# Kernel optimization log

Measured on AMD Instinct MI355X. Metric: run time of the kernel, lower is better.

Reference implementation:

```python
import jax, jax.numpy as jnp
import numpy as np

NEG_SLOPE = 0.01  # F.leaky_relu default
N_NODES = 50000
N_EDGES = 800000
DIMS = [1, 64, 128, 64, 1]


def _lrelu(x):
    return jnp.where(x >= 0, x, NEG_SLOPE * x)


def _gconv(x, src, dst, W, b, n):
    # DGL GraphConv, norm='none': sum-aggregate src features into dst, then linear.
    # (DGL multiplies first when in_feats > out_feats; identical math since sum is linear.)
    if x.shape[1] > W.shape[1]:
        x = x @ W
        return jax.ops.segment_sum(x[src], dst, num_segments=n) + b
    agg = jax.ops.segment_sum(x[src], dst, num_segments=n)  # [n, d_in]
    return agg @ W + b


def setup_inputs() -> dict:
    key = jax.random.key(0)
    ks = jax.random.split(key, 16)
    inp = {
        "in_feat": jax.random.normal(ks[0], (N_NODES, 1), jnp.float32),
        "src": jax.random.randint(ks[1], (N_EDGES,), 0, N_NODES),
        "dst": jax.random.randint(ks[2], (N_EDGES,), 0, N_NODES),
    }
    for i in range(4):
        fi, fo = DIMS[i], DIMS[i + 1]
        scale = (2.0 / (fi + fo)) ** 0.5  # xavier-style
        inp[f"W{i}"] = jax.random.normal(ks[3 + 2 * i], (fi, fo), jnp.float32) * scale
        inp[f"b{i}"] = jax.random.normal(ks[4 + 2 * i], (fo,), jnp.float32) * 0.01
    return inp


def reference(in_feat, src, dst, W0, b0, W1, b1, W2, b2, W3, b3):
    n = in_feat.shape[0]
    h = _lrelu(_gconv(in_feat, src, dst, W0, b0, n))
    h = _lrelu(_gconv(h, src, dst, W1, b1, n))
    h = _lrelu(_gconv(h, src, dst, W2, b2, n))
    h = _lrelu(_gconv(h, src, dst, W3, b3, n))
    return h[1]  # node index 1, shape (1,)
```

## Files before the change

### kernel.cpp

```cpp
#include <hip/hip_runtime.h>

#define N_NODES 50000
#define N_EDGES 800000
#define NE4 (N_EDGES / 4)
#define NMASKW 1568
#define C1MAX 64
#define CAP   16
#define S2MAX 1024
#define DMAX  4096
#define BK    96
#define SB1   ((NE4 + 255) / 256)
#define FGRID 256
#define SUBW  64

#define AS(p, v)  __hip_atomic_store((p), (v), __ATOMIC_RELAXED, __HIP_MEMORY_SCOPE_AGENT)
#define ALD(p)    __hip_atomic_load((p), __ATOMIC_RELAXED, __HIP_MEMORY_SCOPE_AGENT)
#define AADD(p,v) __hip_atomic_fetch_add((p), (v), __ATOMIC_RELAXED, __HIP_MEMORY_SCOPE_AGENT)

__device__ __forceinline__ float lrelu(float v) { return v >= 0.f ? v : 0.01f * v; }
__device__ __forceinline__ bool mtest(const unsigned int* m, int i) {
    return (m[i >> 5] >> (i & 31)) & 1u;
}

__global__ __launch_bounds__(256) void scan1_k(const int4* __restrict__ dst4,
                                               const int* __restrict__ src,
                                               int* __restrict__ e1cnt, int* __restrict__ e1val,
                                               unsigned int* __restrict__ zbase, int zwords) {
    __shared__ int lcnt;
    __shared__ int lval[CAP];
    const int tid = threadIdx.x;
    const int t = blockIdx.x * 256 + tid;
    if (tid == 0) lcnt = 0;
    __syncthreads();
    if (t < zwords) zbase[t] = 0u;
    if (t < NE4) {
        int4 d4 = dst4[t];
        int dv[4] = { d4.x, d4.y, d4.z, d4.w };
#pragma unroll
        for (int k = 0; k < 4; ++k) {
            if (dv[k] == 1) {
                int q = atomicAdd(&lcnt, 1);
                if (q < CAP) lval[q] = src[t * 4 + k];
            }
        }
    }
    __syncthreads();
    int c = lcnt < CAP ? lcnt : CAP;
    if (tid == 0) e1cnt[blockIdx.x] = c;
    if (tid < c) e1val[blockIdx.x * CAP + tid] = lval[tid];
}

__global__ __launch_bounds__(256) void scan2_k(const int4* __restrict__ dst4,
                                               const int* __restrict__ src,
                                               const int* __restrict__ e1cnt,
                                               const int* __restrict__ e1val,
                                               unsigned int* __restrict__ f2m,
                                               int* __restrict__ pos2, int* __restrict__ cnt2,
                                               int2* __restrict__ eD, int* __restrict__ cntD) {
    __shared__ unsigned int msk[NMASKW];
    __shared__ int candN[C1MAX];
    __shared__ int candC;
    const int tid = threadIdx.x;
    for (int k = tid; k < NMASKW; k += 256) msk[k] = 0u;
    if (tid == 0) candC = 0;
    __syncthreads();
    for (int b = tid; b < SB1; b += 256) {
        int c = e1cnt[b]; if (c > CAP) c = CAP;
        for (int i = 0; i < c; ++i) {
            int n = e1val[b * CAP + i];
            unsigned int bit = 1u << (n & 31);
            unsigned int old = atomicOr(&msk[n >> 5], bit);
            if (!(old & bit)) { int q = atomicAdd(&candC, 1); if (q < C1MAX) candN[q] = n; }
        }
    }
    __syncthreads();
    int c1 = candC; if (c1 > C1MAX) c1 = C1MAX;
    int t = blockIdx.x * 256 + tid;
    if (t >= NE4) return;
    int4 d4 = dst4[t];
    int dv[4] = { d4.x, d4.y, d4.z, d4.w };
#pragma unroll
    for (int k = 0; k < 4; ++k) {
        int dd = dv[k];
        if (mtest(msk, dd)) {
            int ss = src[t * 4 + k];
            unsigned int bit = 1u << (ss & 31);
            unsigned int old = atomicOr(&f2m[ss >> 5], bit);
            if (!(old & bit)) {
                int q2 = atomicAdd(cnt2, 1);
                if (q2 < S2MAX) AS(&pos2[ss], q2);
            }
            int r = 0;
            for (int u = 0; u < c1; ++u) r += (candN[u] < dd);
            int q = atomicAdd(cntD, 1);
            if (q < DMAX) {
                unsigned long long ev = (unsigned long long)(unsigned int)ss |
                                        ((unsigned long long)(unsigned int)r << 32);
                AS((unsigned long long*)&eD[q], ev);
            }
        }
    }
}

__global__ __launch_bounds__(256) void scan3_k(const int4* __restrict__ dst4,
                                               const int* __restrict__ src,
                                               const unsigned int* __restrict__ f2m,
                                               unsigned int* __restrict__ f3m,
                                               const int* __restrict__ pos2,
                                               float* __restrict__ agg0,
                                               int* __restrict__ bucket,
                                               int* __restrict__ slotCnt) {
    __shared__ unsigned int msk[NMASKW];
    const int tid = threadIdx.x;
    for (int k = tid; k < NMASKW; k += 256) msk[k] = f2m[k];
    __syncthreads();
    int t = blockIdx.x * 256 + tid;
    if (t >= NE4) return;
    int4 d4 = dst4[t];
    int dv[4] = { d4.x, d4.y, d4.z, d4.w };
#pragma unroll
    for (int k = 0; k < 4; ++k) {
        int dd = dv[k];
        if (mtest(msk, dd)) {
            int ss = src[t * 4 + k];
            unsigned int bit = 1u << (ss & 31);
            unsigned int old = atomicOr(&f3m[ss >> 5], bit);
            if (!(old & bit)) AS(&agg0[ss], 0.f);
            int sl = pos2[dd];
            if ((unsigned)sl < S2MAX) {
                int bi = atomicAdd(&slotCnt[sl], 1);
                if (bi < BK) AS(&bucket[sl * BK + bi], ss);
            }
        }
    }
}

struct P8 {
    const int4* dst4; const int4* src4; const float* x;
    const unsigned int* f3m; float* agg0;
    const int2* eD; const int* cntD; const int* pos2; int2* eDr;
    const int* bucket; const int* slotCnt; const int* cnt2;
    const int* e1cnt; const int* e1val;
    const float* W0; const float* b0; const float* W1; const float* b1;
    const float* W2; const float* b2; const float* W3; const float* b3;
    float* gacc; int* sub; int* top; int* rel; int* subB; int* topB; float* out;
};

__global__ __launch_bounds__(256) void fused8_k(P8 p) {
    __shared__ unsigned int msk[NMASKW];
    __shared__ float xv[128];
    __shared__ float part[256];
    __shared__ float rowA[64];
    __shared__ float rowH[128];
    __shared__ float rowT[64];
    __shared__ float t3s[C1MAX];
    __shared__ int candN[C1MAX];
    __shared__ int candC;
    __shared__ int lflag;
    const int tid = threadIdx.x;
    const int gid = blockIdx.x * 256 + tid;
    const int g = tid >> 6, j = tid & 63;

    int cD = *p.cntD; if (cD > DMAX) cD = DMAX;
    if (gid < cD) {
        int2 e = p.eD[gid];
        int sl = p.pos2[e.x];
        unsigned long long ev =
            (unsigned long long)(unsigned int)((unsigned)sl < S2MAX ? sl : -1) |
            ((unsigned long long)(unsigned int)e.y << 32);
        AS((unsigned long long*)&p.eDr[gid], ev);
    }
    for (int k = tid; k < NMASKW; k += 256) msk[k] = p.f3m[k];
    __syncthreads();
    for (int t = gid; t < NE4; t += FGRID * 256) {
        int4 d4 = p.dst4[t];
        bool m0 = mtest(msk, d4.x), m1 = mtest(msk, d4.y);
        bool m2 = mtest(msk, d4.z), m3 = mtest(msk, d4.w);
        if (m0 | m1 | m2 | m3) {
            int4 s4 = p.src4[t];
            if (m0) atomicAdd(&p.agg0[d4.x], p.x[s4.x]);
            if (m1) atomicAdd(&p.agg0[d4.y], p.x[s4.y]);
            if (m2) atomicAdd(&p.agg0[d4.z], p.x[s4.z]);
            if (m3) atomicAdd(&p.agg0[d4.w], p.x[s4.w]);
        }
    }
    __syncthreads();
    if (tid == 0) {
        int s = blockIdx.x & 7;
        int old = AADD(&p.sub[s * SUBW], 1);
        if (old == (FGRID / 8) - 1) {
            int o2 = AADD(p.top, 1);
            if (o2 == 7) AS(p.rel, 1);
        }
        while (ALD(p.rel) == 0) __builtin_amdgcn_s_sleep(8);
    }
    __syncthreads();

    int c2 = *p.cnt2; if (c2 > S2MAX) c2 = S2MAX;
    const float w0 = p.W0[j], bb0 = p.b0[j];
    for (int b = blockIdx.x; b < c2; b += FGRID) {
        int cnt = p.slotCnt[b]; if (cnt > BK) cnt = BK;
        if (tid < cnt) xv[tid] = p.agg0[p.bucket[b * BK + tid]];
        __syncthreads();
        float racc = 0.f;
        for (int m = g; m < cnt; m += 4) racc += lrelu(xv[m] * w0 + bb0);
        part[tid] = racc;
        __syncthreads();
        if (tid < 64)
            rowA[tid] = part[tid] + part[64 + tid] + part[128 + tid] + part[192 + tid];
        __syncthreads();
        if (tid < 128) {
            float h = p.b1[tid];
#pragma unroll
            for (int k = 0; k < 64; ++k) h += rowA[k] * p.W1[k * 128 + tid];
            rowH[tid] = lrelu(h);
        }
        __syncthreads();
        if (tid < 64) {
            float a2 = 0.f;
#pragma unroll
            for (int k = 0; k < 128; ++k) a2 += rowH[k] * p.W2[k * 64 + tid];
            rowT[tid] = a2;
        }
        __syncthreads();
        for (int base = 0; base < cD; base += 256) {
            int i = base + tid;
            int2 e = make_int2(-1, -1);
            if (i < cD) e = p.eDr[i];
            bool m = (e.x == b);
            unsigned long long bal = __ballot(m);
            while (bal) {
                int bit = __builtin_ctzll(bal); bal &= bal - 1;
                int sl1 = __shfl(e.y, bit, 64);
                if ((unsigned)sl1 < C1MAX)
                    atomicAdd(&p.gacc[sl1 * 64 + j], rowT[j]);
            }
        }
        __syncthreads();
    }

    __syncthreads();
    if (tid == 0) {
        lflag = 0;
        int s = blockIdx.x & 7;
        int old = AADD(&p.subB[s * SUBW], 1);
        if (old == (FGRID / 8) - 1) {
            int o2 = AADD(p.topB, 1);
            lflag = (o2 == 7);
        }
    }
    __syncthreads();
    if (!lflag) return;

    for (int k = tid; k < NMASKW; k += 256) msk[k] = 0u;
    if (tid == 0) candC = 0;
    __syncthreads();
    for (int b = tid; b < SB1; b += 256) {
        int c = p.e1cnt[b]; if (c > CAP) c = CAP;
        for (int i = 0; i < c; ++i) {
            int n = p.e1val[b * CAP + i];
            unsigned int bit = 1u << (n & 31);
            unsigned int old = atomicOr(&msk[n >> 5], bit);
            if (!(old & bit)) { int q = atomicAdd(&candC, 1); if (q < C1MAX) candN[q] = n; }
        }
    }
    __syncthreads();
    int c1 = candC; if (c1 > C1MAX) c1 = C1MAX;
    int widx = tid >> 6;
    for (int q = widx; q < c1; q += 4) {
        int n = candN[q];
        int r = 0;
        for (int u = 0; u < c1; ++u) r += (candN[u] < n);
        float v = lrelu(p.gacc[r * 64 + j] + p.b2[j]) * p.W3[j];
        for (int off = 32; off > 0; off >>= 1) v += __shfl_down(v, off, 64);
        if (j == 0) t3s[r] = v;
    }
    __syncthreads();
    float ssum = 0.f;
    for (int b = tid; b < SB1; b += 256) {
        int c = p.e1cnt[b]; if (c > CAP) c = CAP;
        for (int i = 0; i < c; ++i) {
            int n = p.e1val[b * CAP + i];
            int r = 0;
            for (int u = 0; u < c1; ++u) r += (candN[u] < n);
            ssum += t3s[r];
        }
    }
    part[tid] = ssum;
    __syncthreads();
    for (int off = 128; off > 0; off >>= 1) {
        if (tid < off) part[tid] += part[tid + off];
        __syncthreads();
    }
    if (tid == 0) p.out[0] = lrelu(part[0] + p.b3[0]);
}

extern "C" void kernel_launch(void* const* d_in, const int* in_sizes, int n_in,
                              void* d_out, int out_size, void* d_ws, size_t ws_size,
                              hipStream_t stream) {
    const float* x   = (const float*)d_in[0];
    const int*   src = (const int*)d_in[1];
    const int*   dst = (const int*)d_in[2];
    const float* W0 = (const float*)d_in[3];  const float* b0 = (const float*)d_in[4];
    const float* W1 = (const float*)d_in[5];  const float* b1 = (const float*)d_in[6];
    const float* W2 = (const float*)d_in[7];  const float* b2 = (const float*)d_in[8];
    const float* W3 = (const float*)d_in[9];  const float* b3 = (const float*)d_in[10];
    float* out = (float*)d_out;
    const int4* dst4 = (const int4*)dst;
    const int4* src4 = (const int4*)src;

    char* base = (char*)d_ws;
    size_t off = 0;
    auto take = [&](size_t bytes) { char* q = base + off; off += (bytes + 255) & ~(size_t)255; return q; };
    unsigned int* f2m = (unsigned int*)take(NMASKW * 4);
    unsigned int* f3m = (unsigned int*)take(NMASKW * 4);
    int* cnt2  = (int*)take(4);
    int* cntD  = (int*)take(4);
    int* top   = (int*)take(4);
    int* rel   = (int*)take(4);
    int* topB  = (int*)take(4);
    int* sub   = (int*)take((size_t)8 * SUBW * 4);
    int* subB  = (int*)take((size_t)8 * SUBW * 4);
    int* slotCnt = (int*)take((size_t)S2MAX * 4);
    float* gacc  = (float*)take((size_t)C1MAX * 64 * 4);
    int zwords = (int)(off / 4);
    float* agg0   = (float*)take((size_t)N_NODES * 4);
    int*   e1cnt  = (int*)take((size_t)SB1 * 4);
    int*   e1val  = (int*)take((size_t)SB1 * CAP * 4);
    int2*  eD     = (int2*)take((size_t)DMAX * 8);
    int2*  eDr    = (int2*)take((size_t)DMAX * 8);
    int*   bucket = (int*)take((size_t)S2MAX * BK * 4);
    int*   pos2   = (int*)take((size_t)N_NODES * 4);

    scan1_k<<<SB1, 256, 0, stream>>>(dst4, src, e1cnt, e1val, (unsigned int*)base, zwords);
    scan2_k<<<SB1, 256, 0, stream>>>(dst4, src, e1cnt, e1val, f2m, pos2, cnt2, eD, cntD);
    scan3_k<<<SB1, 256, 0, stream>>>(dst4, src, f2m, f3m, pos2, agg0, bucket, slotCnt);

    P8 hp;
    hp.dst4 = dst4; hp.src4 = src4; hp.x = x;
    hp.f3m = f3m; hp.agg0 = agg0;
    hp.eD = eD; hp.cntD = cntD; hp.pos2 = pos2; hp.eDr = eDr;
    hp.bucket = bucket; hp.slotCnt = slotCnt; hp.cnt2 = cnt2;
    hp.e1cnt = e1cnt; hp.e1val = e1val;
    hp.W0 = W0; hp.b0 = b0; hp.W1 = W1; hp.b1 = b1;
    hp.W2 = W2; hp.b2 = b2; hp.W3 = W3; hp.b3 = b3;
    hp.gacc = gacc; hp.sub = sub; hp.top = top; hp.rel = rel;
    hp.subB = subB; hp.topB = topB; hp.out = out;
    fused8_k<<<FGRID, 256, 0, stream>>>(hp);
}
```

Before: 139.4 us.

## Split edge aggregation into separate kernel, replacing in-kernel grid barrier

The layer-0 masked edge aggregation and the eDr remap move out of the fused kernel into a new full-grid kernel, scan4_k. This removes the spin-wait grid barrier that separated that phase from the per-bucket MLP phase. The aggregation now runs with one thread per int4 chunk across all blocks instead of a 256-block grid-stride loop, which should help parallelism. In exchange it adds one kernel launch and its boundary overhead.

```diff
diff --git a/kernel.cpp b/kernel.cpp
--- a/kernel.cpp
+++ b/kernel.cpp
@@ -14,7 +14,6 @@
 #define SUBW  64
 
 #define AS(p, v)  __hip_atomic_store((p), (v), __ATOMIC_RELAXED, __HIP_MEMORY_SCOPE_AGENT)
-#define ALD(p)    __hip_atomic_load((p), __ATOMIC_RELAXED, __HIP_MEMORY_SCOPE_AGENT)
 #define AADD(p,v) __hip_atomic_fetch_add((p), (v), __ATOMIC_RELAXED, __HIP_MEMORY_SCOPE_AGENT)
 
 __device__ __forceinline__ float lrelu(float v) { return v >= 0.f ? v : 0.01f * v; }
@@ -135,18 +134,53 @@
     }
 }
 
-struct P8 {
-    const int4* dst4; const int4* src4; const float* x;
-    const unsigned int* f3m; float* agg0;
-    const int2* eD; const int* cntD; const int* pos2; int2* eDr;
-    const int* bucket; const int* slotCnt; const int* cnt2;
-    const int* e1cnt; const int* e1val;
+__global__ __launch_bounds__(256) void scan4_k(const int4* __restrict__ dst4,
+                                               const int4* __restrict__ src4,
+                                               const float* __restrict__ x,
+                                               const unsigned int* __restrict__ f3m,
+                                               float* __restrict__ agg0,
+                                               const int2* __restrict__ eD,
+                                               const int* __restrict__ cntD,
+                                               const int* __restrict__ pos2,
+                                               int2* __restrict__ eDr) {
+    __shared__ unsigned int msk[NMASKW];
+    int g = blockIdx.x * 256 + threadIdx.x;
+    {
+        int cD = *cntD; if (cD > DMAX) cD = DMAX;
+        if (g < cD) {
+            int2 e = eD[g];
+            int sl = pos2[e.x];
+            unsigned long long ev =
+                (unsigned long long)(unsigned int)((unsigned)sl < S2MAX ? sl : -1) |
+                ((unsigned long long)(unsigned int)e.y << 32);
+            AS((unsigned long long*)&eDr[g], ev);
+        }
+    }
+    for (int k = threadIdx.x; k < NMASKW; k += 256) msk[k] = f3m[k];
+    __syncthreads();
+    if (g >= NE4) return;
+    int4 d4 = dst4[g];
+    bool m0 = mtest(msk, d4.x), m1 = mtest(msk, d4.y);
+    bool m2 = mtest(msk, d4.z), m3 = mtest(msk, d4.w);
+    if (m0 | m1 | m2 | m3) {
+        int4 s4 = src4[g];
+        if (m0) atomicAdd(&agg0[d4.x], x[s4.x]);
+        if (m1) atomicAdd(&agg0[d4.y], x[s4.y]);
+        if (m2) atomicAdd(&agg0[d4.z], x[s4.z]);
+        if (m3) atomicAdd(&agg0[d4.w], x[s4.w]);
+    }
+}
+
+struct P10 {
+    const int* bucket; const int* slotCnt; const float* agg0;
     const float* W0; const float* b0; const float* W1; const float* b1;
     const float* W2; const float* b2; const float* W3; const float* b3;
-    float* gacc; int* sub; int* top; int* rel; int* subB; int* topB; float* out;
+    const int* cnt2; const int2* eDr; const int* cntD;
+    const int* e1cnt; const int* e1val;
+    float* gacc; int* sub; int* top; float* out;
 };
 
-__global__ __launch_bounds__(256) void fused8_k(P8 p) {
+__global__ __launch_bounds__(256) void fused10_k(P10 p) {
     __shared__ unsigned int msk[NMASKW];
     __shared__ float xv[128];
     __shared__ float part[256];
@@ -158,46 +192,11 @@
     __shared__ int candC;
     __shared__ int lflag;
     const int tid = threadIdx.x;
-    const int gid = blockIdx.x * 256 + tid;
     const int g = tid >> 6, j = tid & 63;
-
+    int c2 = *p.cnt2; if (c2 > S2MAX) c2 = S2MAX;
     int cD = *p.cntD; if (cD > DMAX) cD = DMAX;
-    if (gid < cD) {
-        int2 e = p.eD[gid];
-        int sl = p.pos2[e.x];
-        unsigned long long ev =
-            (unsigned long long)(unsigned int)((unsigned)sl < S2MAX ? sl : -1) |
-            ((unsigned long long)(unsigned int)e.y << 32);
-        AS((unsigned long long*)&p.eDr[gid], ev);
-    }
-    for (int k = tid; k < NMASKW; k += 256) msk[k] = p.f3m[k];
-    __syncthreads();
-    for (int t = gid; t < NE4; t += FGRID * 256) {
-        int4 d4 = p.dst4[t];
-        bool m0 = mtest(msk, d4.x), m1 = mtest(msk, d4.y);
-        bool m2 = mtest(msk, d4.z), m3 = mtest(msk, d4.w);
-        if (m0 | m1 | m2 | m3) {
-            int4 s4 = p.src4[t];
-            if (m0) atomicAdd(&p.agg0[d4.x], p.x[s4.x]);
-            if (m1) atomicAdd(&p.agg0[d4.y], p.x[s4.y]);
-            if (m2) atomicAdd(&p.agg0[d4.z], p.x[s4.z]);
-            if (m3) atomicAdd(&p.agg0[d4.w], p.x[s4.w]);
-        }
-    }
-    __syncthreads();
-    if (tid == 0) {
-        int s = blockIdx.x & 7;
-        int old = AADD(&p.sub[s * SUBW], 1);
-        if (old == (FGRID / 8) - 1) {
-            int o2 = AADD(p.top, 1);
-            if (o2 == 7) AS(p.rel, 1);
-        }
-        while (ALD(p.rel) == 0) __builtin_amdgcn_s_sleep(8);
-    }
-    __syncthreads();
-
-    int c2 = *p.cnt2; if (c2 > S2MAX) c2 = S2MAX;
     const float w0 = p.W0[j], bb0 = p.b0[j];
+
     for (int b = blockIdx.x; b < c2; b += FGRID) {
         int cnt = p.slotCnt[b]; if (cnt > BK) cnt = BK;
         if (tid < cnt) xv[tid] = p.agg0[p.bucket[b * BK + tid]];
@@ -243,9 +242,9 @@
     if (tid == 0) {
         lflag = 0;
         int s = blockIdx.x & 7;
-        int old = AADD(&p.subB[s * SUBW], 1);
+        int old = AADD(&p.sub[s * SUBW], 1);
         if (old == (FGRID / 8) - 1) {
-            int o2 = AADD(p.topB, 1);
+            int o2 = AADD(p.top, 1);
             lflag = (o2 == 7);
         }
     }
@@ -317,10 +316,7 @@
     int* cnt2  = (int*)take(4);
     int* cntD  = (int*)take(4);
     int* top   = (int*)take(4);
-    int* rel   = (int*)take(4);
-    int* topB  = (int*)take(4);
     int* sub   = (int*)take((size_t)8 * SUBW * 4);
-    int* subB  = (int*)take((size_t)8 * SUBW * 4);
     int* slotCnt = (int*)take((size_t)S2MAX * 4);
     float* gacc  = (float*)take((size_t)C1MAX * 64 * 4);
     int zwords = (int)(off / 4);
@@ -335,16 +331,14 @@
     scan1_k<<<SB1, 256, 0, stream>>>(dst4, src, e1cnt, e1val, (unsigned int*)base, zwords);
     scan2_k<<<SB1, 256, 0, stream>>>(dst4, src, e1cnt, e1val, f2m, pos2, cnt2, eD, cntD);
     scan3_k<<<SB1, 256, 0, stream>>>(dst4, src, f2m, f3m, pos2, agg0, bucket, slotCnt);
-
-    P8 hp;
-    hp.dst4 = dst4; hp.src4 = src4; hp.x = x;
-    hp.f3m = f3m; hp.agg0 = agg0;
-    hp.eD = eD; hp.cntD = cntD; hp.pos2 = pos2; hp.eDr = eDr;
-    hp.bucket = bucket; hp.slotCnt = slotCnt; hp.cnt2 = cnt2;
-    hp.e1cnt = e1cnt; hp.e1val = e1val;
+    scan4_k<<<SB1, 256, 0, stream>>>(dst4, src4, x, f3m, agg0, eD, cntD, pos2, eDr);
+
+    P10 hp;
+    hp.bucket = bucket; hp.slotCnt = slotCnt; hp.agg0 = agg0;
     hp.W0 = W0; hp.b0 = b0; hp.W1 = W1; hp.b1 = b1;
     hp.W2 = W2; hp.b2 = b2; hp.W3 = W3; hp.b3 = b3;
-    hp.gacc = gacc; hp.sub = sub; hp.top = top; hp.rel = rel;
-    hp.subB = subB; hp.topB = topB; hp.out = out;
-    fused8_k<<<FGRID, 256, 0, stream>>>(hp);
-}
+    hp.cnt2 = cnt2; hp.eDr = eDr; hp.cntD = cntD;
+    hp.e1cnt = e1cnt; hp.e1val = e1val;
+    hp.gacc = gacc; hp.sub = sub; hp.top = top; hp.out = out;
+    fused10_k<<<FGRID, 256, 0, stream>>>(hp);
+}
```

New measurement: 132.9 us. -4.6%, faster.
